# Performance work log

Measured on AMD Instinct MI355X. Metric: run time of the kernel, lower is better.

Reference implementation:

```python
import jax, jax.numpy as jnp
import numpy as np

# ---- synthetic softmax-tree (matches read_softmax_tree output format) ----
R, B, K = 16, 2, 8  # root group size, child groups per root node, lower-level group size
ROOT_SIZE = 0       # (number of root groups) - 1
THRESHOLD = 0.5
MAXG = 16           # max group size (root group has 16, others 8)
MAXCH = 2           # max subgroups pushed per node (child_sizes+1)
STACK = 16          # safe bound >= module's computed stack_size


def _build_tree():
    group_offsets, group_sizes = [0], [R]
    child, child_sizes = [], []
    # level-1 (root) nodes: each has B child groups starting at group 1+B*i
    for i in range(R):
        child.append(1 + B * i)
        child_sizes.append(B - 1)
    n_l2 = R * B * K
    for gi in range(R * B):
        group_offsets.append(R + gi * K)
        group_sizes.append(K)
    # level-2 nodes: each has a single leaf group
    l3_first_group = 1 + R * B
    for j in range(n_l2):
        child.append(l3_first_group + j)
        child_sizes.append(0)
    for gj in range(n_l2):
        group_offsets.append(R + n_l2 + gj * K)
        group_sizes.append(K)
    # level-3 leaf nodes
    for _ in range(n_l2 * K):
        child.append(-1)
        child_sizes.append(0)
    return (np.asarray(group_offsets, np.int32), np.asarray(group_sizes, np.int32),
            np.asarray(child, np.int32), np.asarray(child_sizes, np.int32))


def setup_inputs() -> dict:
    key = jax.random.key(0)
    k1, k2 = jax.random.split(key)
    go, gs, ch, cs = _build_tree()
    node_count = int(go[-1] + gs[-1])  # 2320
    N, H, W = 16, 64, 64
    conf = jax.random.uniform(k1, (N, node_count, H, W), dtype=jnp.float32)
    obj = jax.random.uniform(k2, (N, H, W), dtype=jnp.float32)
    return {
        "conf": conf, "obj": obj,
        "group_offsets": jnp.asarray(go), "group_sizes": jnp.asarray(gs),
        "child": jnp.asarray(ch), "child_sizes": jnp.asarray(cs),
    }


def _smt_predict(conf, obj, group_offsets, group_sizes, child, child_sizes):
    # Stack-based DFS softmax-tree path selection with threshold pruning.
    # conf: [N, C, H, W] group-softmaxed probabilities; obj: [N, H, W].
    N, C, H, W = conf.shape
    inner = H * W
    # one lane per (sample, spatial location)
    conf2 = conf.reshape(N, C, inner).transpose(0, 2, 1).reshape(N * inner, C)
    obj2 = obj.reshape(N * inner)
    # pad channel dim so dynamic_slice windows never clip/shift
    confp = jnp.concatenate(
        [conf2, jnp.full((N * inner, MAXG), -jnp.inf, conf.dtype)], axis=1)

    lane = jnp.arange(MAXCH, dtype=jnp.int32)
    garange = jnp.arange(MAXG)

    def traverse(c_loc, o_loc):
        top = jnp.zeros((C,), conf.dtype)
        sg = jnp.zeros((STACK,), jnp.int32)          # group stack
        sp = jnp.zeros((STACK,), conf.dtype)          # parent path prob
        spa = jnp.full((STACK,), -1, jnp.int32)       # parent argmax node
        nroot = ROOT_SIZE + 1
        sg = sg.at[:nroot].set(jnp.arange(nroot, dtype=jnp.int32))
        sp = sp.at[:nroot].set(o_loc)                 # path prob starts at objectness

        def cond(st):
            return st[4] > 0

        def body(st):
            top, sg, sp, spa, ptr = st
            ptr = ptr - 1
            g, pp, pa = sg[ptr], sp[ptr], spa[ptr]
            off, size = group_offsets[g], group_sizes[g]
            win = jax.lax.dynamic_slice(c_loc, (off,), (MAXG,))
            win = jnp.where(garange < size, win, -jnp.inf)
            j = jnp.argmax(win)
            p = pp * win[j]                  # cumulative path probability
            amax = off + j
            c, cs_n = child[amax], child_sizes[amax]
            above = p > THRESHOLD
            # leaf hit -> write p at argmax; pruned -> write parent prob at parent node
            widx = jnp.where(above, amax, pa)
            wval = jnp.where(above, p, pp)
            do_w = jnp.where(above, c < 0, pa >= 0)
            safe = jnp.maximum(widx, 0)
            top = top.at[safe].set(jnp.where(do_w, wval, top[safe]))
            # descend: push subgroups c .. c+child_sizes of the argmax node
            npush = jnp.where(above & (c >= 0), cs_n + 1, 0).astype(jnp.int32)
            pm = lane < npush
            ii = ptr + lane
            sg = sg.at[ii].set(jnp.where(pm, c + lane, sg[ii]))
            sp = sp.at[ii].set(jnp.where(pm, p, sp[ii]))
            spa = spa.at[ii].set(jnp.where(pm, amax, spa[ii]))
            return (top, sg, sp, spa, ptr + npush)

        top, *_ = jax.lax.while_loop(cond, body, (top, sg, sp, spa, jnp.int32(nroot)))
        return jnp.concatenate([top, jnp.max(top)[None]])  # append_max channel

    out = jax.vmap(traverse)(confp, obj2)  # [N*inner, C+1]
    return out.reshape(N, inner, C + 1).transpose(0, 2, 1).reshape(N, C + 1, H, W)


def reference(conf, obj, group_offsets, group_sizes, child, child_sizes):
    return _smt_predict(conf, obj, group_offsets, group_sizes, child, child_sizes)
```

## Files before the change

kernel.cpp:

```cpp
#include <hip/hip_runtime.h>
#include <cmath>


#define SMT_THRESHOLD 0.5f
#define SMT_MAXG 16
#define SMT_INNER_LOG2 12
#define SMT_INNER 4096

typedef float floatx4 __attribute__((ext_vector_type(4)));

__global__ __launch_bounds__(256) void smt_zero_kernel(
    float* __restrict__ out, long long n_elems) {
    long long n4 = n_elems >> 2;
    floatx4* __restrict__ out4 = (floatx4*)out;
    long long stride = (long long)gridDim.x * blockDim.x;
    long long tid = (long long)blockIdx.x * blockDim.x + threadIdx.x;
    floatx4 z = {0.0f, 0.0f, 0.0f, 0.0f};
    for (long long i = tid; i < n4; i += stride) {
        __builtin_nontemporal_store(z, out4 + i);
    }
    long long rem = n_elems & 3;
    if (tid < rem) out[(n4 << 2) + tid] = 0.0f;
}

__device__ inline void group_argmax(const float* __restrict__ cbase, int off,
                                    int size, float& best, int& bj) {
    float v[SMT_MAXG];
#pragma unroll
    for (int j = 0; j < SMT_MAXG; ++j) {
        v[j] = (j < size) ? cbase[(long long)(off + j) << SMT_INNER_LOG2]
                          : -INFINITY;
    }
    best = v[0];
    bj = 0;
#pragma unroll
    for (int j = 1; j < SMT_MAXG; ++j) {
        if (v[j] > best) { best = v[j]; bj = j; }
    }
}

__global__ __launch_bounds__(256) void smt_traverse_kernel(
    const float* __restrict__ conf,
    const float* __restrict__ obj,
    const int* __restrict__ go,
    const int* __restrict__ gs,
    const int* __restrict__ child,
    const int* __restrict__ csize,
    float* __restrict__ out,
    int C, int total) {
    int lane = blockIdx.x * blockDim.x + threadIdx.x;
    if (lane >= total) return;
    int hw = lane & (SMT_INNER - 1);
    long long nCinner = (long long)(lane - hw) * C;
    const float* cbase = conf + nCinner + hw;
    float* obase = out + nCinner +
                   (long long)(lane >> SMT_INNER_LOG2) * SMT_INNER + hw;

    float o = obj[lane];
    float maxtop = 0.0f;

    int off0 = go[0], sz0 = gs[0];
    float best0; int j0;
    group_argmax(cbase, off0, sz0, best0, j0);
    float p0 = o * best0;
    int amax0 = off0 + j0;
    if (p0 > SMT_THRESHOLD) {
        int c0 = child[amax0];
        int cs0 = csize[amax0];
        if (c0 < 0) {
            obase[(long long)amax0 << SMT_INNER_LOG2] = p0;
            maxtop = fmaxf(maxtop, p0);
        } else {
#pragma unroll
            for (int l = 0; l < 2; ++l) {
                if (l <= cs0) {
                    int g2 = c0 + l;
                    int off2 = go[g2], sz2 = gs[g2];
                    float best2; int j2;
                    group_argmax(cbase, off2, sz2, best2, j2);
                    float p2 = p0 * best2;
                    int amax2 = off2 + j2;
                    int c2 = child[amax2];
                    int cs2 = csize[amax2];
                    if (p2 > SMT_THRESHOLD) {
                        if (c2 < 0) {
                            obase[(long long)amax2 << SMT_INNER_LOG2] = p2;
                            maxtop = fmaxf(maxtop, p2);
                        } else {
#pragma unroll
                            for (int m = 0; m < 2; ++m) {
                                if (m <= cs2) {
                                    int g3 = c2 + m;
                                    int off3 = go[g3], sz3 = gs[g3];
                                    float best3; int j3;
                                    group_argmax(cbase, off3, sz3, best3, j3);
                                    float p3 = p2 * best3;
                                    int amax3 = off3 + j3;
                                    int c3 = child[amax3];
                                    if (p3 > SMT_THRESHOLD) {
                                        if (c3 < 0) {
                                            obase[(long long)amax3
                                                  << SMT_INNER_LOG2] = p3;
                                            maxtop = fmaxf(maxtop, p3);
                                        }
                                    } else {
                                        obase[(long long)amax2
                                              << SMT_INNER_LOG2] = p2;
                                        maxtop = fmaxf(maxtop, p2);
                                    }
                                }
                            }
                        }
                    } else {
                        obase[(long long)amax0 << SMT_INNER_LOG2] = p0;
                        maxtop = fmaxf(maxtop, p0);
                    }
                }
            }
        }
    }
    obase[(long long)C << SMT_INNER_LOG2] = maxtop;
}

extern "C" void kernel_launch(void* const* d_in, const int* in_sizes, int n_in,
                              void* d_out, int out_size, void* d_ws, size_t ws_size,
                              hipStream_t stream) {
    const float* conf = (const float*)d_in[0];
    const float* obj  = (const float*)d_in[1];
    const int* go     = (const int*)d_in[2];
    const int* gs     = (const int*)d_in[3];
    const int* child  = (const int*)d_in[4];
    const int* csize  = (const int*)d_in[5];
    float* out = (float*)d_out;

    const int C = in_sizes[4];
    const int total = in_sizes[1];

    long long n_elems = (long long)out_size;
    smt_zero_kernel<<<2048, 256, 0, stream>>>(out, n_elems);

    int tblocks = (total + 255) / 256;
    smt_traverse_kernel<<<tblocks, 256, 0, stream>>>(
        conf, obj, go, gs, child, csize, out, C, total);
}
```

Before: 907.4 us.

## Overlap output zero-fill with traversal via fused kernel and deferred scatter

The zero-fill of the large output and the tree traversal now run in one launch, split by block index, so the fill and the conf reads can overlap. Traversal results (up to two winners plus the max) go to a workspace, and a small scatter kernel then writes them into the zeroed output. The fill also drops its nontemporal stores in favour of plain stores. This adds an extra launch and workspace traffic, and the fallback path depends on whether enough workspace is provided.

```diff
diff --git a/kernel.cpp b/kernel.cpp
--- a/kernel.cpp
+++ b/kernel.cpp
@@ -6,8 +6,148 @@
 #define SMT_MAXG 16
 #define SMT_INNER_LOG2 12
 #define SMT_INNER 4096
+#define FILL_BLOCKS 2048
 
 typedef float floatx4 __attribute__((ext_vector_type(4)));
+
+__device__ inline void group_argmax(const float* __restrict__ cbase, int off,
+                                    int size, float& best, int& bj) {
+    float v[SMT_MAXG];
+#pragma unroll
+    for (int j = 0; j < SMT_MAXG; ++j) {
+        v[j] = (j < size) ? cbase[(long long)(off + j) << SMT_INNER_LOG2]
+                          : -INFINITY;
+    }
+    best = v[0];
+    bj = 0;
+#pragma unroll
+    for (int j = 1; j < SMT_MAXG; ++j) {
+        if (v[j] > best) { best = v[j]; bj = j; }
+    }
+}
+
+__device__ inline void traverse_pixel(const float* __restrict__ cbase, float o,
+                                      const int* __restrict__ go,
+                                      const int* __restrict__ gs,
+                                      const int* __restrict__ child,
+                                      const int* __restrict__ csize,
+                                      int& cnt, int& c0, float& v0, int& c1,
+                                      float& v1, float& maxtop) {
+    cnt = 0;
+    c0 = 0; v0 = 0.0f; c1 = 0; v1 = 0.0f;
+    maxtop = 0.0f;
+
+    int off0 = go[0], sz0 = gs[0];
+    float best0; int j0;
+    group_argmax(cbase, off0, sz0, best0, j0);
+    float p0 = o * best0;
+    int amax0 = off0 + j0;
+    if (p0 > SMT_THRESHOLD) {
+        int ch0 = child[amax0];
+        int cs0 = csize[amax0];
+        if (ch0 < 0) {
+            if (cnt == 0) { c0 = amax0; v0 = p0; } else { c1 = amax0; v1 = p0; }
+            ++cnt;
+            maxtop = fmaxf(maxtop, p0);
+        } else {
+#pragma unroll
+            for (int l = 0; l < 2; ++l) {
+                if (l <= cs0) {
+                    int g2 = ch0 + l;
+                    int off2 = go[g2], sz2 = gs[g2];
+                    float best2; int j2;
+                    group_argmax(cbase, off2, sz2, best2, j2);
+                    float p2 = p0 * best2;
+                    int amax2 = off2 + j2;
+                    int ch2 = child[amax2];
+                    int cs2 = csize[amax2];
+                    int wi = -1; float wv = 0.0f;
+                    if (p2 > SMT_THRESHOLD) {
+                        if (ch2 < 0) {
+                            wi = amax2; wv = p2;
+                        } else {
+#pragma unroll
+                            for (int m = 0; m < 2; ++m) {
+                                if (m <= cs2) {
+                                    int g3 = ch2 + m;
+                                    int off3 = go[g3], sz3 = gs[g3];
+                                    float best3; int j3;
+                                    group_argmax(cbase, off3, sz3, best3, j3);
+                                    float p3 = p2 * best3;
+                                    int amax3 = off3 + j3;
+                                    int ch3 = child[amax3];
+                                    if (p3 > SMT_THRESHOLD) {
+                                        if (ch3 < 0) { wi = amax3; wv = p3; }
+                                    } else {
+                                        wi = amax2; wv = p2;
+                                    }
+                                }
+                            }
+                        }
+                    } else {
+                        wi = amax0; wv = p0;
+                    }
+                    if (wi >= 0 && cnt < 2) {
+                        if (cnt == 0) { c0 = wi; v0 = wv; }
+                        else          { c1 = wi; v1 = wv; }
+                        ++cnt;
+                        maxtop = fmaxf(maxtop, wv);
+                    }
+                }
+            }
+        }
+    }
+}
+
+__global__ __launch_bounds__(256) void smt_fused_kernel(
+    const float* __restrict__ conf, const float* __restrict__ obj,
+    const int* __restrict__ go, const int* __restrict__ gs,
+    const int* __restrict__ child, const int* __restrict__ csize,
+    float* __restrict__ out, long long n_elems,
+    float* __restrict__ wmax, int* __restrict__ wcnt, int* __restrict__ wc0,
+    float* __restrict__ wv0, int* __restrict__ wc1, float* __restrict__ wv1,
+    int C, int total) {
+    if (blockIdx.x < FILL_BLOCKS) {
+        long long n4 = n_elems >> 2;
+        floatx4* __restrict__ out4 = (floatx4*)out;
+        long long stride = (long long)FILL_BLOCKS * blockDim.x;
+        long long tid = (long long)blockIdx.x * blockDim.x + threadIdx.x;
+        floatx4 z = {0.0f, 0.0f, 0.0f, 0.0f};
+        for (long long i = tid; i < n4; i += stride) out4[i] = z;
+        long long rem = n_elems & 3;
+        if (tid < rem) out[(n4 << 2) + tid] = 0.0f;
+        return;
+    }
+    int lane = (blockIdx.x - FILL_BLOCKS) * blockDim.x + threadIdx.x;
+    if (lane >= total) return;
+    int hw = lane & (SMT_INNER - 1);
+    long long nCinner = (long long)(lane - hw) * C;
+    const float* cbase = conf + nCinner + hw;
+    float o = obj[lane];
+    int cnt, ci0, ci1; float cv0, cv1, mt;
+    traverse_pixel(cbase, o, go, gs, child, csize, cnt, ci0, cv0, ci1, cv1, mt);
+    wcnt[lane] = cnt;
+    wc0[lane] = ci0; wv0[lane] = cv0;
+    wc1[lane] = ci1; wv1[lane] = cv1;
+    wmax[lane] = mt;
+}
+
+__global__ __launch_bounds__(256) void smt_scatter_kernel(
+    const float* __restrict__ wmax, const int* __restrict__ wcnt,
+    const int* __restrict__ wc0, const float* __restrict__ wv0,
+    const int* __restrict__ wc1, const float* __restrict__ wv1,
+    float* __restrict__ out, int C, int total) {
+    int lane = blockIdx.x * blockDim.x + threadIdx.x;
+    if (lane >= total) return;
+    int hw = lane & (SMT_INNER - 1);
+    long long nCinner = (long long)(lane - hw) * C;
+    float* obase = out + nCinner +
+                   (long long)(lane >> SMT_INNER_LOG2) * SMT_INNER + hw;
+    obase[(long long)C << SMT_INNER_LOG2] = wmax[lane];
+    int cnt = wcnt[lane];
+    if (cnt > 0) obase[(long long)wc0[lane] << SMT_INNER_LOG2] = wv0[lane];
+    if (cnt > 1) obase[(long long)wc1[lane] << SMT_INNER_LOG2] = wv1[lane];
+}
 
 __global__ __launch_bounds__(256) void smt_zero_kernel(
     float* __restrict__ out, long long n_elems) {
@@ -16,38 +156,16 @@
     long long stride = (long long)gridDim.x * blockDim.x;
     long long tid = (long long)blockIdx.x * blockDim.x + threadIdx.x;
     floatx4 z = {0.0f, 0.0f, 0.0f, 0.0f};
-    for (long long i = tid; i < n4; i += stride) {
-        __builtin_nontemporal_store(z, out4 + i);
-    }
+    for (long long i = tid; i < n4; i += stride) out4[i] = z;
     long long rem = n_elems & 3;
     if (tid < rem) out[(n4 << 2) + tid] = 0.0f;
 }
 
-__device__ inline void group_argmax(const float* __restrict__ cbase, int off,
-                                    int size, float& best, int& bj) {
-    float v[SMT_MAXG];
-#pragma unroll
-    for (int j = 0; j < SMT_MAXG; ++j) {
-        v[j] = (j < size) ? cbase[(long long)(off + j) << SMT_INNER_LOG2]
-                          : -INFINITY;
-    }
-    best = v[0];
-    bj = 0;
-#pragma unroll
-    for (int j = 1; j < SMT_MAXG; ++j) {
-        if (v[j] > best) { best = v[j]; bj = j; }
-    }
-}
-
-__global__ __launch_bounds__(256) void smt_traverse_kernel(
-    const float* __restrict__ conf,
-    const float* __restrict__ obj,
-    const int* __restrict__ go,
-    const int* __restrict__ gs,
-    const int* __restrict__ child,
-    const int* __restrict__ csize,
-    float* __restrict__ out,
-    int C, int total) {
+__global__ __launch_bounds__(256) void smt_traverse_direct_kernel(
+    const float* __restrict__ conf, const float* __restrict__ obj,
+    const int* __restrict__ go, const int* __restrict__ gs,
+    const int* __restrict__ child, const int* __restrict__ csize,
+    float* __restrict__ out, int C, int total) {
     int lane = blockIdx.x * blockDim.x + threadIdx.x;
     if (lane >= total) return;
     int hw = lane & (SMT_INNER - 1);
@@ -55,71 +173,12 @@
     const float* cbase = conf + nCinner + hw;
     float* obase = out + nCinner +
                    (long long)(lane >> SMT_INNER_LOG2) * SMT_INNER + hw;
-
     float o = obj[lane];
-    float maxtop = 0.0f;
-
-    int off0 = go[0], sz0 = gs[0];
-    float best0; int j0;
-    group_argmax(cbase, off0, sz0, best0, j0);
-    float p0 = o * best0;
-    int amax0 = off0 + j0;
-    if (p0 > SMT_THRESHOLD) {
-        int c0 = child[amax0];
-        int cs0 = csize[amax0];
-        if (c0 < 0) {
-            obase[(long long)amax0 << SMT_INNER_LOG2] = p0;
-            maxtop = fmaxf(maxtop, p0);
-        } else {
-#pragma unroll
-            for (int l = 0; l < 2; ++l) {
-                if (l <= cs0) {
-                    int g2 = c0 + l;
-                    int off2 = go[g2], sz2 = gs[g2];
-                    float best2; int j2;
-                    group_argmax(cbase, off2, sz2, best2, j2);
-                    float p2 = p0 * best2;
-                    int amax2 = off2 + j2;
-                    int c2 = child[amax2];
-                    int cs2 = csize[amax2];
-                    if (p2 > SMT_THRESHOLD) {
-                        if (c2 < 0) {
-                            obase[(long long)amax2 << SMT_INNER_LOG2] = p2;
-                            maxtop = fmaxf(maxtop, p2);
-                        } else {
-#pragma unroll
-                            for (int m = 0; m < 2; ++m) {
-                                if (m <= cs2) {
-                                    int g3 = c2 + m;
-                                    int off3 = go[g3], sz3 = gs[g3];
-                                    float best3; int j3;
-                                    group_argmax(cbase, off3, sz3, best3, j3);
-                                    float p3 = p2 * best3;
-                                    int amax3 = off3 + j3;
-                                    int c3 = child[amax3];
-                                    if (p3 > SMT_THRESHOLD) {
-                                        if (c3 < 0) {
-                                            obase[(long long)amax3
-                                                  << SMT_INNER_LOG2] = p3;
-                                            maxtop = fmaxf(maxtop, p3);
-                                        }
-                                    } else {
-                                        obase[(long long)amax2
-                                              << SMT_INNER_LOG2] = p2;
-                                        maxtop = fmaxf(maxtop, p2);
-                                    }
-                                }
-                            }
-                        }
-                    } else {
-                        obase[(long long)amax0 << SMT_INNER_LOG2] = p0;
-                        maxtop = fmaxf(maxtop, p0);
-                    }
-                }
-            }
-        }
-    }
-    obase[(long long)C << SMT_INNER_LOG2] = maxtop;
+    int cnt, ci0, ci1; float cv0, cv1, mt;
+    traverse_pixel(cbase, o, go, gs, child, csize, cnt, ci0, cv0, ci1, cv1, mt);
+    if (cnt > 0) obase[(long long)ci0 << SMT_INNER_LOG2] = cv0;
+    if (cnt > 1) obase[(long long)ci1 << SMT_INNER_LOG2] = cv1;
+    obase[(long long)C << SMT_INNER_LOG2] = mt;
 }
 
 extern "C" void kernel_launch(void* const* d_in, const int* in_sizes, int n_in,
@@ -135,11 +194,28 @@
 
     const int C = in_sizes[4];
     const int total = in_sizes[1];
-
     long long n_elems = (long long)out_size;
-    smt_zero_kernel<<<2048, 256, 0, stream>>>(out, n_elems);
-
-    int tblocks = (total + 255) / 256;
-    smt_traverse_kernel<<<tblocks, 256, 0, stream>>>(
-        conf, obj, go, gs, child, csize, out, C, total);
-}
+
+    size_t ws_needed = (size_t)total * 6 * sizeof(float);
+    if (ws_size >= ws_needed && d_ws != nullptr) {
+        float* ws = (float*)d_ws;
+        float* wmax = ws;
+        int*   wcnt = (int*)(ws + total);
+        int*   wc0  = (int*)(ws + 2 * (size_t)total);
+        float* wv0  = ws + 3 * (size_t)total;
+        int*   wc1  = (int*)(ws + 4 * (size_t)total);
+        float* wv1  = ws + 5 * (size_t)total;
+
+        int trav_blocks = (total + 255) / 256;
+        smt_fused_kernel<<<FILL_BLOCKS + trav_blocks, 256, 0, stream>>>(
+            conf, obj, go, gs, child, csize, out, n_elems,
+            wmax, wcnt, wc0, wv0, wc1, wv1, C, total);
+        smt_scatter_kernel<<<trav_blocks, 256, 0, stream>>>(
+            wmax, wcnt, wc0, wv0, wc1, wv1, out, C, total);
+    } else {
+        smt_zero_kernel<<<FILL_BLOCKS, 256, 0, stream>>>(out, n_elems);
+        int tblocks = (total + 255) / 256;
+        smt_traverse_direct_kernel<<<tblocks, 256, 0, stream>>>(
+            conf, obj, go, gs, child, csize, out, C, total);
+    }
+}
```

Result: no change. 898.4 us (-1.0%).
